# Performance work log

Hardware: AMD Instinct MI355X
Metric: run time of the kernel (lower is better)

The kernel has to match this reference:

```python
import jax, jax.numpy as jnp
import numpy as np

INPUT_SZ = 1024
HIDDEN_SZ = 1024


def setup_inputs() -> dict:
    key = jax.random.key(0)
    k1, k2, k3, k4, k5, k6 = jax.random.split(key, 6)
    s = 1.0 / np.sqrt(INPUT_SZ)
    x_batch = jax.random.normal(k1, (8, 2048, INPUT_SZ), dtype=jnp.float32)
    lin_w = jax.random.normal(k2, (INPUT_SZ, INPUT_SZ), dtype=jnp.float32) * s  # nn.Linear weight (out,in)
    lin_b = jax.random.normal(k3, (INPUT_SZ,), dtype=jnp.float32) * s
    W_q = jax.random.normal(k4, (INPUT_SZ, HIDDEN_SZ), dtype=jnp.float32) * s
    W_k = jax.random.normal(k5, (INPUT_SZ, HIDDEN_SZ), dtype=jnp.float32) * s
    W_v = jax.random.normal(k6, (INPUT_SZ, HIDDEN_SZ), dtype=jnp.float32) * s
    return {"x_batch": x_batch, "lin_w": lin_w, "lin_b": lin_b,
            "W_q": W_q, "W_k": W_k, "W_v": W_v}


def reference(x_batch, lin_w, lin_b, W_q, W_k, W_v):
    # x_batch: [B, S, D]. Prefill path (empty kv_cache of shape (2,)).
    B, S, D = x_batch.shape
    x = jnp.einsum('bsd,ed->bse', x_batch, lin_w) + lin_b  # nn.Linear: x @ W.T + b
    Q = jnp.einsum('bsd,dh->bsh', x, W_q)
    K = jnp.einsum('bsd,dh->bsh', x, W_k)
    V = jnp.einsum('bsd,dh->bsh', x, W_v)
    current_cache = jnp.stack([K, V])  # [2, B, S, H]
    I = jnp.einsum('bqh,bkh->bqk', Q, K)  # NOTE: no 1/sqrt(d) scaling, per original
    causal_mask = jnp.triu(jnp.ones((S, S), dtype=bool), k=1)  # True above diagonal
    I = jnp.where(causal_mask[None, :, :], -jnp.inf, I)
    F = jnp.einsum('bqk,bkh->bqh', jax.nn.softmax(I, axis=-1), V)
    return (F, current_cache)
```

## Files before the change

### kernel.cpp

```cpp
#include <hip/hip_runtime.h>
#include <cstdint>
#include <cstddef>
#include <cmath>


typedef short bf16x8 __attribute__((ext_vector_type(8)));
typedef float f32x4 __attribute__((ext_vector_type(4)));

__device__ __forceinline__ unsigned short f2bf(float f) {
    unsigned u = __float_as_uint(f);
    return (unsigned short)((u + 0x7fffu + ((u >> 16) & 1u)) >> 16);
}
__device__ __forceinline__ float bf2f(unsigned short h) {
    return __uint_as_float(((unsigned)h) << 16);
}

#define GLDS(gp, lp)                                                                \
    __builtin_amdgcn_global_load_lds((const __attribute__((address_space(1))) void*)(gp), \
                                     (__attribute__((address_space(3))) void*)(lp), 16, 0, 0)

#define PACK_BATCH ((size_t)136 * 16384)


__global__ __launch_bounds__(256)
void cvt_split(const float* __restrict__ in, unsigned short* __restrict__ h,
               unsigned short* __restrict__ l, size_t n4)
{
    size_t i = (size_t)blockIdx.x * blockDim.x + threadIdx.x;
    size_t stride = (size_t)gridDim.x * blockDim.x;
    for (; i < n4; i += stride) {
        float4 v = ((const float4*)in)[i];
        unsigned short h0 = f2bf(v.x), h1 = f2bf(v.y), h2 = f2bf(v.z), h3 = f2bf(v.w);
        uint2 hp, lp;
        hp.x = (unsigned)h0 | ((unsigned)h1 << 16);
        hp.y = (unsigned)h2 | ((unsigned)h3 << 16);
        lp.x = (unsigned)f2bf(v.x - bf2f(h0)) | ((unsigned)f2bf(v.y - bf2f(h1)) << 16);
        lp.y = (unsigned)f2bf(v.z - bf2f(h2)) | ((unsigned)f2bf(v.w - bf2f(h3)) << 16);
        ((uint2*)h)[i] = hp;
        ((uint2*)l)[i] = lp;
    }
}

template<bool PAIR>
__global__ __launch_bounds__(256)
void cvt_split_T(const float* __restrict__ in, unsigned short* __restrict__ hT,
                 unsigned short* __restrict__ lT, int R, int C,
                 size_t inBatch, size_t outBatch)
{
    __shared__ float tile[64][65];
    in += (size_t)blockIdx.z * inBatch;
    hT += (size_t)blockIdx.z * outBatch;
    const int c0 = blockIdx.x * 64, r0 = blockIdx.y * 64;
    const int tx = threadIdx.x & 63, ty = threadIdx.x >> 6;
    for (int i = ty; i < 64; i += 4)
        tile[i][tx] = in[(size_t)(r0 + i) * C + c0 + tx];
    __syncthreads();
    for (int i = ty; i < 64; i += 4) {
        float v = tile[tx][i];
        unsigned short hh = f2bf(v);
        size_t off = (size_t)(c0 + i) * R + r0 + tx;
        hT[off] = hh;
        if (PAIR) (lT + (size_t)blockIdx.z * outBatch)[off] = f2bf(v - bf2f(hh));
    }
}


template<bool SPLIT, bool BIAS, bool QKT, bool OUTF, bool OUTH, bool OUTL>
__global__ __launch_bounds__(512, 2)
void gemm256(const unsigned short* __restrict__ Ah, const unsigned short* __restrict__ Al,
             const unsigned short* __restrict__ Bh, const unsigned short* __restrict__ Bl,
             const float* __restrict__ bias,
             float* __restrict__ C, float* __restrict__ C7,
             unsigned short* __restrict__ Ch, unsigned short* __restrict__ Cl,
             int K, int ldA, int ldB, int ldC, int nbx,
             size_t aBatch, size_t bBatch)
{
    int row0, col0, batch = 0;
    if (QKT) {
        const int bid = blockIdx.x;
        batch = bid & 7;
        const int ti = bid >> 3;
        int r = (int)((sqrtf(8.f * (float)ti + 1.f) - 1.f) * 0.5f);
        while (((r + 1) * (r + 2)) / 2 <= ti) ++r;
        while ((r * (r + 1)) / 2 > ti) --r;
        const int c = ti - (r * (r + 1)) / 2;
        row0 = r * 256; col0 = c * 256;
        Ah += (size_t)batch * aBatch; Bh += (size_t)batch * bBatch;
        if (SPLIT) { Al += (size_t)batch * aBatch; Bl += (size_t)batch * bBatch; }
    } else {
        const int bid = blockIdx.x;
        const int chunk = gridDim.x >> 3;
        const int lb = (bid & 7) * chunk + (bid >> 3);
        row0 = (lb / nbx) * 256; col0 = (lb % nbx) * 256;
    }

    constexpr int PL = 8192;
    constexpr int BUF = SPLIT ? 32768 : 16384;
    __shared__ unsigned short sm[SPLIT ? 65536 : 32768];

    const int t = threadIdx.x, wave = t >> 6, lane = t & 63;
    const int wr = wave >> 2, wc = wave & 3;
    const int mrow = lane & 15, kg = lane >> 4;
    const int c0 = wave * 2, c1 = wave * 2 + 1;

    const size_t aOff0 = (size_t)(row0 + c0 * 16 + mrow) * ldA + kg * 8;
    const size_t aOff1 = (size_t)(row0 + c1 * 16 + mrow) * ldA + kg * 8;
    const size_t bOff0 = (size_t)(col0 + c0 * 16 + mrow) * ldB + kg * 8;
    const size_t bOff1 = (size_t)(col0 + c1 * 16 + mrow) * ldB + kg * 8;

    f32x4 acc[8][4] = {};
    const int nt = K / 32;

#define STAGE256(step, bb)                                                   \
    do {                                                                     \
        unsigned short* db = sm + (bb);                                      \
        const size_t kof = (size_t)(step) * 32;                              \
        GLDS(Ah + aOff0 + kof, db + c0 * 512);                               \
        GLDS(Ah + aOff1 + kof, db + c1 * 512);                               \
        GLDS(Bh + bOff0 + kof, db + (SPLIT ? 2 * PL : PL) + c0 * 512);       \
        GLDS(Bh + bOff1 + kof, db + (SPLIT ? 2 * PL : PL) + c1 * 512);       \
        if (SPLIT) {                                                         \
            GLDS(Al + aOff0 + kof, db + PL + c0 * 512);                      \
            GLDS(Al + aOff1 + kof, db + PL + c1 * 512);                      \
            GLDS(Bl + bOff0 + kof, db + 3 * PL + c0 * 512);                  \
            GLDS(Bl + bOff1 + kof, db + 3 * PL + c1 * 512);                  \
        }                                                                    \
    } while (0)

    STAGE256(0, 0);
    __syncthreads();

    for (int ts = 0; ts < nt; ++ts) {
        unsigned short* sb = sm + (ts & 1) * BUF;
        if (ts + 1 < nt) STAGE256(ts + 1, ((ts + 1) & 1) * BUF);
        bf16x8 bh[4], bl[4];
        #pragma unroll
        for (int j = 0; j < 4; ++j) {
            bh[j] = *(const bf16x8*)(sb + (SPLIT ? 2 * PL : PL) + (wc * 4 + j) * 512 + lane * 8);
            if (SPLIT) bl[j] = *(const bf16x8*)(sb + 3 * PL + (wc * 4 + j) * 512 + lane * 8);
        }
        #pragma unroll
        for (int i = 0; i < 8; ++i) {
            bf16x8 ah = *(const bf16x8*)(sb + (wr * 8 + i) * 512 + lane * 8);
            bf16x8 al;
            if (SPLIT) al = *(const bf16x8*)(sb + PL + (wr * 8 + i) * 512 + lane * 8);
            __builtin_amdgcn_s_setprio(1);
            #pragma unroll
            for (int j = 0; j < 4; ++j) {
                acc[i][j] = __builtin_amdgcn_mfma_f32_16x16x32_bf16(ah, bh[j], acc[i][j], 0, 0, 0);
                if (SPLIT) {
                    acc[i][j] = __builtin_amdgcn_mfma_f32_16x16x32_bf16(ah, bl[j], acc[i][j], 0, 0, 0);
                    acc[i][j] = __builtin_amdgcn_mfma_f32_16x16x32_bf16(al, bh[j], acc[i][j], 0, 0, 0);
                }
            }
            __builtin_amdgcn_s_setprio(0);
        }
        __syncthreads();
    }
#undef STAGE256

    float* Cout = C;
    if (QKT) Cout = (batch == 7) ? C7 : C + (size_t)batch * PACK_BATCH;
    const int rb = (lane >> 4) * 4, cl = lane & 15;
    #pragma unroll
    for (int j = 0; j < 4; ++j) {
        const int col = col0 + wc * 64 + j * 16 + cl;
        const float bv = BIAS ? bias[col] : 0.f;
        #pragma unroll
        for (int i = 0; i < 8; ++i) {
            const int rw = row0 + wr * 128 + i * 16 + rb;
            #pragma unroll
            for (int r = 0; r < 4; ++r) {
                const int row = rw + r;
                float v = acc[i][j][r];
                if (BIAS) v += bv;
                if (QKT) {
                    if (col > row) v = -__builtin_huge_valf();
                    const int rblk = row >> 7, cblk = col >> 7;
                    if (rblk >= cblk) {
                        const size_t off = ((size_t)(((rblk * (rblk + 1)) >> 1) + cblk) << 14)
                                         + ((size_t)(row & 127) << 7) + (size_t)(col & 127);
                        Cout[off] = v;
                    }
                } else {
                    const size_t off = (size_t)row * ldC + col;
                    if (OUTF) Cout[off] = v;
                    if (OUTH) {
                        unsigned short hh = f2bf(v);
                        Ch[off] = hh;
                        if (OUTL) Cl[off] = f2bf(v - bf2f(hh));
                    }
                }
            }
        }
    }
}


template<bool SPLIT, bool BIAS, bool CMASK, bool CK, bool OUTF, bool OUTH, bool OUTL,
         bool PACKC, bool PACKA>
__global__ __launch_bounds__(256)
void gemm_bf16(const unsigned short* __restrict__ Ah, const unsigned short* __restrict__ Al,
               const unsigned short* __restrict__ Bh, const unsigned short* __restrict__ Bl,
               const float* __restrict__ bias,
               float* __restrict__ C, float* __restrict__ C7,
               unsigned short* __restrict__ Ch, unsigned short* __restrict__ Cl,
               int K, int ldA, int ldB, int ldC,
               size_t aBatch, size_t bBatch, size_t cBatch)
{
    const int row0 = blockIdx.y * 128, col0 = blockIdx.x * 128;
    if (CMASK && col0 > row0 + 127) return;

    const int bz = blockIdx.z;
    if (aBatch) { Ah += (size_t)bz * aBatch; if (SPLIT) Al += (size_t)bz * aBatch; }
    if (bBatch) { Bh += (size_t)bz * bBatch; if (SPLIT) Bl += (size_t)bz * bBatch; }
    if (cBatch) { C += (size_t)bz * cBatch; }

    extern __shared__ __align__(16) unsigned short smd[];
    unsigned short* sAh = smd;
    unsigned short* sBh = smd + 4096;
    unsigned short* sAl = smd + 8192;
    unsigned short* sBl = smd + 12288;

    const int t = threadIdx.x;
    const int wave = t >> 6, lane = t & 63;
    const int wr = wave >> 1, wc = wave & 1;
    const int mrow = lane & 15, kg = lane >> 4;

    int kEnd = K;
    if (CK) kEnd = min(K, row0 + 128);

    f32x4 acc[4][4] = {};

    const int c0 = wave * 2, c1 = wave * 2 + 1;
    size_t aOff0, aOff1;
    if (PACKA) {
        const int rblk = row0 >> 7;
        const size_t baseA = (((size_t)bz * 136) + (size_t)((rblk * (rblk + 1)) >> 1)) << 14;
        aOff0 = baseA + (size_t)(c0 * 16 + mrow) * 128 + kg * 8;
        aOff1 = baseA + (size_t)(c1 * 16 + mrow) * 128 + kg * 8;
    } else {
        aOff0 = (size_t)(row0 + c0 * 16 + mrow) * ldA + kg * 8;
        aOff1 = (size_t)(row0 + c1 * 16 + mrow) * ldA + kg * 8;
    }
    const size_t bOff0 = (size_t)(col0 + c0 * 16 + mrow) * ldB + kg * 8;
    const size_t bOff1 = (size_t)(col0 + c1 * 16 + mrow) * ldB + kg * 8;

    for (int k0 = 0; k0 < kEnd; k0 += 32) {
        const size_t aK = PACKA ? ((((size_t)(k0 >> 7)) << 14) | (size_t)(k0 & 127))
                                : (size_t)k0;
        GLDS(Ah + aOff0 + aK, sAh + c0 * 512);
        GLDS(Ah + aOff1 + aK, sAh + c1 * 512);
        GLDS(Bh + bOff0 + k0, sBh + c0 * 512);
        GLDS(Bh + bOff1 + k0, sBh + c1 * 512);
        if (SPLIT) {
            GLDS(Al + aOff0 + aK, sAl + c0 * 512);
            GLDS(Al + aOff1 + aK, sAl + c1 * 512);
            GLDS(Bl + bOff0 + k0, sBl + c0 * 512);
            GLDS(Bl + bOff1 + k0, sBl + c1 * 512);
        }
        __syncthreads();

        bf16x8 afh[4], bfh[4], afl[4], bfl[4];
        #pragma unroll
        for (int i = 0; i < 4; ++i) {
            afh[i] = *(const bf16x8*)(sAh + (wr * 4 + i) * 512 + lane * 8);
            bfh[i] = *(const bf16x8*)(sBh + (wc * 4 + i) * 512 + lane * 8);
            if (SPLIT) {
                afl[i] = *(const bf16x8*)(sAl + (wr * 4 + i) * 512 + lane * 8);
                bfl[i] = *(const bf16x8*)(sBl + (wc * 4 + i) * 512 + lane * 8);
            }
        }
        #pragma unroll
        for (int i = 0; i < 4; ++i)
            #pragma unroll
            for (int j = 0; j < 4; ++j) {
                acc[i][j] = __builtin_amdgcn_mfma_f32_16x16x32_bf16(afh[i], bfh[j], acc[i][j], 0, 0, 0);
                if (SPLIT) {
                    acc[i][j] = __builtin_amdgcn_mfma_f32_16x16x32_bf16(afh[i], bfl[j], acc[i][j], 0, 0, 0);
                    acc[i][j] = __builtin_amdgcn_mfma_f32_16x16x32_bf16(afl[i], bfh[j], acc[i][j], 0, 0, 0);
                }
            }
        __syncthreads();
    }

    float* Cout = C;
    size_t cbase = 0;
    if (PACKC) {
        const int rblk = row0 >> 7, cblk = col0 >> 7;
        Cout = (bz == 7) ? C7 : C + (size_t)bz * PACK_BATCH;
        cbase = ((size_t)((rblk * (rblk + 1)) >> 1) + (size_t)cblk) << 14;
    }
    const int rb = (lane >> 4) * 4;
    const int cl = lane & 15;
    #pragma unroll
    for (int j = 0; j < 4; ++j) {
        const int col = col0 + wc * 64 + j * 16 + cl;
        float bv = BIAS ? bias[col] : 0.f;
        #pragma unroll
        for (int i = 0; i < 4; ++i) {
            const int rw = row0 + wr * 64 + i * 16 + rb;
            #pragma unroll
            for (int r = 0; r < 4; ++r) {
                const int row = rw + r;
                float v = acc[i][j][r];
                if (BIAS) v += bv;
                if (CMASK && col > row) v = -__builtin_huge_valf();
                const size_t off = PACKC
                    ? (cbase + (size_t)(row - row0) * 128 + (size_t)(col - col0))
                    : ((size_t)row * ldC + col);
                if (OUTF) Cout[off] = v;
                if (OUTH) {
                    unsigned short hh = f2bf(v);
                    Ch[off] = hh;
                    if (OUTL) Cl[off] = f2bf(v - bf2f(hh));
                }
            }
        }
    }
}

__global__ __launch_bounds__(256)
void softmax_p_packed(const float* __restrict__ SF, const float* __restrict__ S7,
                      unsigned short* __restrict__ P)
{
    const int q = blockIdx.x, b = blockIdx.y;
    const int rblk = q >> 7, tri = (rblk * (rblk + 1)) >> 1;
    const size_t rowoff = ((size_t)tri << 14) + (size_t)(q & 127) * 128;
    const float* rowb = ((b == 7) ? S7 : SF + (size_t)b * PACK_BATCH) + rowoff;
    unsigned short* prow = P + (size_t)b * PACK_BATCH + rowoff;
    const int kend = rblk * 128 + 128;
    const int t = threadIdx.x;
    __shared__ float red[4];

    float m = -__builtin_huge_valf();
    for (int k = t; k < kend; k += 256)
        m = fmaxf(m, rowb[(((size_t)(k >> 7)) << 14) + (k & 127)]);
    #pragma unroll
    for (int off = 32; off; off >>= 1) m = fmaxf(m, __shfl_down(m, off, 64));
    if ((t & 63) == 0) red[t >> 6] = m;
    __syncthreads();
    m = fmaxf(fmaxf(red[0], red[1]), fmaxf(red[2], red[3]));
    __syncthreads();

    float e[8];
    float s = 0.f;
    int i = 0;
    for (int k = t; k < kend; k += 256, ++i) {
        float v = __expf(rowb[(((size_t)(k >> 7)) << 14) + (k & 127)] - m);
        e[i] = v;
        s += v;
    }
    #pragma unroll
    for (int off = 32; off; off >>= 1) s += __shfl_down(s, off, 64);
    if ((t & 63) == 0) red[t >> 6] = s;
    __syncthreads();
    s = red[0] + red[1] + red[2] + red[3];
    const float inv = 1.0f / s;
    i = 0;
    for (int k = t; k < kend; k += 256, ++i)
        prow[(((size_t)(k >> 7)) << 14) + (k & 127)] = f2bf(e[i] * inv);
}

#define TILE 64
#define KT 16
#define LDP (TILE + 4)
template<bool BT, bool BIAS, bool CMASK, bool CK>
__global__ __launch_bounds__(256)
void gemm_f32(const float* __restrict__ A, const float* __restrict__ B,
              const float* __restrict__ bias, float* __restrict__ C,
              int M, int N, int K, size_t sA, size_t sB, size_t sC)
{
    const int bm = blockIdx.y, bn = blockIdx.x;
    const int row0 = bm * TILE, col0 = bn * TILE;
    if (CMASK && col0 > row0 + (TILE - 1)) return;
    A += (size_t)blockIdx.z * sA; B += (size_t)blockIdx.z * sB; C += (size_t)blockIdx.z * sC;
    __shared__ float As[KT][LDP];
    __shared__ float Bs[KT][LDP];
    const int t = threadIdx.x;
    const int tx = t & 15, ty = t >> 4;
    const int lm = t >> 2, lk = (t & 3) << 2;
    int kEnd = K;
    if (CK) kEnd = min(K, row0 + TILE);
    float acc[4][4] = {};
    for (int k0 = 0; k0 < kEnd; k0 += KT) {
        {
            float4 a = *(const float4*)(A + (size_t)(row0 + lm) * K + (k0 + lk));
            As[lk + 0][lm] = a.x; As[lk + 1][lm] = a.y; As[lk + 2][lm] = a.z; As[lk + 3][lm] = a.w;
        }
        if (BT) {
            float4 b = *(const float4*)(B + (size_t)(col0 + lm) * K + (k0 + lk));
            Bs[lk + 0][lm] = b.x; Bs[lk + 1][lm] = b.y; Bs[lk + 2][lm] = b.z; Bs[lk + 3][lm] = b.w;
        } else {
            const int bk = t >> 4, bn4 = (t & 15) << 2;
            *(float4*)&Bs[bk][bn4] = *(const float4*)(B + (size_t)(k0 + bk) * N + (col0 + bn4));
        }
        __syncthreads();
        #pragma unroll
        for (int kk = 0; kk < KT; ++kk) {
            float av[4], bv[4];
            *(float4*)av = *(const float4*)&As[kk][ty << 2];
            *(float4*)bv = *(const float4*)&Bs[kk][tx << 2];
            #pragma unroll
            for (int i = 0; i < 4; ++i)
                #pragma unroll
                for (int j = 0; j < 4; ++j) acc[i][j] = fmaf(av[i], bv[j], acc[i][j]);
        }
        __syncthreads();
    }
    #pragma unroll
    for (int i = 0; i < 4; ++i) {
        const int r = row0 + (ty << 2) + i;
        float4 o; float* po = &o.x;
        #pragma unroll
        for (int j = 0; j < 4; ++j) {
            const int c = col0 + (tx << 2) + j;
            float v = acc[i][j];
            if (BIAS) v += bias[c];
            if (CMASK && c > r) v = -__builtin_huge_valf();
            po[j] = v;
        }
        *(float4*)(C + (size_t)r * N + col0 + (tx << 2)) = o;
    }
}
__global__ __launch_bounds__(256)
void softmax_causal(float* __restrict__ Sc, size_t batchStride, int ncols)
{
    const int q = blockIdx.x;
    float* row = Sc + (size_t)blockIdx.y * batchStride + (size_t)q * ncols;
    const int kend = (q & ~63) + 64;
    const int t = threadIdx.x;
    __shared__ float red[4];
    float m = -__builtin_huge_valf();
    for (int k = t; k < kend; k += 256) m = fmaxf(m, row[k]);
    #pragma unroll
    for (int off = 32; off; off >>= 1) m = fmaxf(m, __shfl_down(m, off, 64));
    if ((t & 63) == 0) red[t >> 6] = m;
    __syncthreads();
    m = fmaxf(fmaxf(red[0], red[1]), fmaxf(red[2], red[3]));
    __syncthreads();
    float e[8]; float s = 0.f; int i = 0;
    for (int k = t; k < kend; k += 256, ++i) { float v = __expf(row[k] - m); e[i] = v; s += v; }
    #pragma unroll
    for (int off = 32; off; off >>= 1) s += __shfl_down(s, off, 64);
    if ((t & 63) == 0) red[t >> 6] = s;
    __syncthreads();
    s = red[0] + red[1] + red[2] + red[3];
    const float inv = 1.0f / s;
    i = 0;
    for (int k = t; k < kend; k += 256, ++i) row[k] = e[i] * inv;
}


extern "C" void kernel_launch(void* const* d_in, const int* in_sizes, int n_in,
                              void* d_out, int out_size, void* d_ws, size_t ws_size,
                              hipStream_t stream)
{
    const float* x_batch = (const float*)d_in[0];
    const float* lin_w   = (const float*)d_in[1];
    const float* lin_b   = (const float*)d_in[2];
    const float* W_q     = (const float*)d_in[3];
    const float* W_k     = (const float*)d_in[4];
    const float* W_v     = (const float*)d_in[5];

    constexpr int Bn = 8, S = 2048, D = 1024;
    constexpr size_t MS = (size_t)Bn * S;
    constexpr size_t NE = MS * (size_t)D;
    constexpr size_t SB = (size_t)S * D;

    float* out = (float*)d_out;
    float* Fo = out;
    float* Kc = out + NE;
    float* Vc = out + 2 * NE;

    const size_t needFast = NE * 2 * 2ull
                          + NE * 2 * 2ull
                          + 14680064ull;

    if (ws_size >= needFast) {
        unsigned short* Qh  = (unsigned short*)d_ws;
        unsigned short* Ql  = Qh + NE;
        unsigned short* Kh  = Ql + NE;
        unsigned short* Kl  = Kh + NE;
        unsigned short* X   = Kl + NE;
        unsigned short* lwh = X,            *lwl = X + 1048576;
        unsigned short* wqh = X + 2097152,  *wql = X + 3145728;
        unsigned short* wkh = X + 4194304,  *wkl = X + 5242880;
        unsigned short* wvh = X + 6291456;
        float*          S7f = (float*)X;
        float*          SF  = Fo;
        unsigned short* Ph  = Qh;
        unsigned short* VhT = Kh;

        unsigned short* xbh = (unsigned short*)Kc;
        unsigned short* xbl = xbh + NE;
        unsigned short* xh  = (unsigned short*)Fo;
        unsigned short* xl  = xh + NE;

        const dim3 blk(256);
        const dim3 blk512(512);

        cvt_split<<<4096, blk, 0, stream>>>(x_batch, xbh, xbl, NE / 4);
        cvt_split<<<512,  blk, 0, stream>>>(lin_w, lwh, lwl, (size_t)D * D / 4);
        cvt_split_T<true ><<<dim3(16, 16, 1), blk, 0, stream>>>(W_q, wqh, wql, D, D, 0, 0);
        cvt_split_T<true ><<<dim3(16, 16, 1), blk, 0, stream>>>(W_k, wkh, wkl, D, D, 0, 0);
        cvt_split_T<false><<<dim3(16, 16, 1), blk, 0, stream>>>(W_v, wvh, nullptr, D, D, 0, 0);

        gemm256<true, true, false, false, true, true><<<dim3(256), blk512, 0, stream>>>(
            xbh, xbl, lwh, lwl, lin_b, nullptr, nullptr, xh, xl, D, D, D, D, 4, 0, 0);
        gemm256<true, false, false, false, true, true><<<dim3(256), blk512, 0, stream>>>(
            xh, xl, wqh, wql, nullptr, nullptr, nullptr, Qh, Ql, D, D, D, D, 4, 0, 0);
        gemm256<true, false, false, true, true, true><<<dim3(256), blk512, 0, stream>>>(
            xh, xl, wkh, wkl, nullptr, Kc, nullptr, Kh, Kl, D, D, D, D, 4, 0, 0);
        gemm256<false, false, false, true, false, false><<<dim3(256), blk512, 0, stream>>>(
            xh, nullptr, wvh, nullptr, nullptr, Vc, nullptr, nullptr, nullptr,
            D, D, D, D, 4, 0, 0);

        gemm256<true, false, true, true, false, false><<<dim3(288), blk512, 0, stream>>>(
            Qh, Ql, Kh, Kl, nullptr, SF, S7f, nullptr, nullptr,
            D, D, D, 128, 1, SB, SB);

        softmax_p_packed<<<dim3(S, Bn), blk, 0, stream>>>(SF, S7f, Ph);

        cvt_split_T<false><<<dim3(D / 64, S / 64, Bn), blk, 0, stream>>>(
            Vc, VhT, nullptr, S, D, SB, SB);

        gemm_bf16<false, false, false, true, true, false, false, false, true>
            <<<dim3(D / 128, S / 128, Bn), blk, 16384, stream>>>(
                Ph, nullptr, VhT, nullptr, nullptr,
                Fo, nullptr, nullptr, nullptr, S, 128, S, D, 0, SB, SB);
    } else {
        float* x  = Fo;
        float* Q  = (float*)d_ws;
        float* Sc = Q + NE;
        const dim3 blk(256);
        const dim3 gBig(D / TILE, MS / TILE, 1);
        gemm_f32<true, true, false, false><<<gBig, blk, 0, stream>>>(
            x_batch, lin_w, lin_b, x, (int)MS, D, D, 0, 0, 0);
        gemm_f32<false, false, false, false><<<gBig, blk, 0, stream>>>(
            x, W_q, nullptr, Q, (int)MS, D, D, 0, 0, 0);
        gemm_f32<false, false, false, false><<<gBig, blk, 0, stream>>>(
            x, W_k, nullptr, Kc, (int)MS, D, D, 0, 0, 0);
        gemm_f32<false, false, false, false><<<gBig, blk, 0, stream>>>(
            x, W_v, nullptr, Vc, (int)MS, D, D, 0, 0, 0);
        for (int b = 0; b < Bn; ++b) {
            const float* Qb = Q  + (size_t)b * SB;
            const float* Kb = Kc + (size_t)b * SB;
            const float* Vb = Vc + (size_t)b * SB;
            float*       Fb = Fo + (size_t)b * SB;
            gemm_f32<true, false, true, false><<<dim3(S / TILE, S / TILE, 1), blk, 0, stream>>>(
                Qb, Kb, nullptr, Sc, S, S, D, 0, 0, 0);
            softmax_causal<<<dim3(S, 1, 1), blk, 0, stream>>>(Sc, 0, S);
            gemm_f32<false, false, false, true><<<dim3(D / TILE, S / TILE, 1), blk, 0, stream>>>(
                Sc, Vb, nullptr, Fb, S, D, S, 0, 0, 0);
        }
    }
}
```

Before: 1.063 ms.

## Split GEMM k-step into phases interleaving LDS reads, prefetch and MFMA with barriers

After: 1.077 ms. About the same (+1.3%).

```diff
diff --git a/kernel.cpp b/kernel.cpp
--- a/kernel.cpp
+++ b/kernel.cpp
@@ -110,54 +110,98 @@
 
     f32x4 acc[8][4] = {};
     const int nt = K / 32;
-
-#define STAGE256(step, bb)                                                   \
+    constexpr int NPH = SPLIT ? 4 : 2;
+    constexpr int RPP = 8 / NPH;
+
+#define STAGE_A(step, db)                                                    \
     do {                                                                     \
-        unsigned short* db = sm + (bb);                                      \
         const size_t kof = (size_t)(step) * 32;                              \
-        GLDS(Ah + aOff0 + kof, db + c0 * 512);                               \
-        GLDS(Ah + aOff1 + kof, db + c1 * 512);                               \
-        GLDS(Bh + bOff0 + kof, db + (SPLIT ? 2 * PL : PL) + c0 * 512);       \
-        GLDS(Bh + bOff1 + kof, db + (SPLIT ? 2 * PL : PL) + c1 * 512);       \
+        GLDS(Ah + aOff0 + kof, (db) + c0 * 512);                             \
+        GLDS(Ah + aOff1 + kof, (db) + c1 * 512);                             \
         if (SPLIT) {                                                         \
-            GLDS(Al + aOff0 + kof, db + PL + c0 * 512);                      \
-            GLDS(Al + aOff1 + kof, db + PL + c1 * 512);                      \
-            GLDS(Bl + bOff0 + kof, db + 3 * PL + c0 * 512);                  \
-            GLDS(Bl + bOff1 + kof, db + 3 * PL + c1 * 512);                  \
+            GLDS(Al + aOff0 + kof, (db) + PL + c0 * 512);                    \
+            GLDS(Al + aOff1 + kof, (db) + PL + c1 * 512);                    \
         }                                                                    \
     } while (0)
-
-    STAGE256(0, 0);
-    __syncthreads();
+#define STAGE_B(step, db)                                                    \
+    do {                                                                     \
+        const size_t kof = (size_t)(step) * 32;                              \
+        unsigned short* bp = (db) + (SPLIT ? 2 * PL : PL);                   \
+        GLDS(Bh + bOff0 + kof, bp + c0 * 512);                               \
+        GLDS(Bh + bOff1 + kof, bp + c1 * 512);                               \
+        if (SPLIT) {                                                         \
+            GLDS(Bl + bOff0 + kof, bp + PL + c0 * 512);                      \
+            GLDS(Bl + bOff1 + kof, bp + PL + c1 * 512);                      \
+        }                                                                    \
+    } while (0)
+
+    STAGE_A(0, sm);
+    STAGE_B(0, sm);
+    asm volatile("s_waitcnt vmcnt(0)" ::: "memory");
+    __builtin_amdgcn_sched_barrier(0);
+    __builtin_amdgcn_s_barrier();
+    __builtin_amdgcn_sched_barrier(0);
 
     for (int ts = 0; ts < nt; ++ts) {
         unsigned short* sb = sm + (ts & 1) * BUF;
-        if (ts + 1 < nt) STAGE256(ts + 1, ((ts + 1) & 1) * BUF);
+        unsigned short* nb = sm + ((ts + 1) & 1) * BUF;
+        const unsigned short* sA0 = sb;
+        const unsigned short* sB0 = sb + (SPLIT ? 2 * PL : PL);
+        const bool pf = (ts + 1 < nt);
+
         bf16x8 bh[4], bl[4];
         #pragma unroll
-        for (int j = 0; j < 4; ++j) {
-            bh[j] = *(const bf16x8*)(sb + (SPLIT ? 2 * PL : PL) + (wc * 4 + j) * 512 + lane * 8);
-            if (SPLIT) bl[j] = *(const bf16x8*)(sb + 3 * PL + (wc * 4 + j) * 512 + lane * 8);
-        }
-        #pragma unroll
-        for (int i = 0; i < 8; ++i) {
-            bf16x8 ah = *(const bf16x8*)(sb + (wr * 8 + i) * 512 + lane * 8);
-            bf16x8 al;
-            if (SPLIT) al = *(const bf16x8*)(sb + PL + (wr * 8 + i) * 512 + lane * 8);
+        for (int ph = 0; ph < NPH; ++ph) {
+            bf16x8 ah[RPP], al[RPP];
+            if (ph == 0) {
+                #pragma unroll
+                for (int j = 0; j < 4; ++j) {
+                    bh[j] = *(const bf16x8*)(sB0 + (wc * 4 + j) * 512 + lane * 8);
+                    if (SPLIT) bl[j] = *(const bf16x8*)(sB0 + PL + (wc * 4 + j) * 512 + lane * 8);
+                }
+            }
+            #pragma unroll
+            for (int u = 0; u < RPP; ++u) {
+                const int ri = wr * 8 + ph * RPP + u;
+                ah[u] = *(const bf16x8*)(sA0 + ri * 512 + lane * 8);
+                if (SPLIT) al[u] = *(const bf16x8*)(sA0 + PL + ri * 512 + lane * 8);
+            }
+            if (ph == 0 && pf) {
+                STAGE_A(ts + 1, nb);
+                if (!SPLIT) STAGE_B(ts + 1, nb);
+            }
+            if (SPLIT && ph == 1 && pf) STAGE_B(ts + 1, nb);
+
+            __builtin_amdgcn_sched_barrier(0);
+            __builtin_amdgcn_s_barrier();
+            asm volatile("s_waitcnt lgkmcnt(0)" ::: "memory");
+            __builtin_amdgcn_sched_barrier(0);
+
             __builtin_amdgcn_s_setprio(1);
             #pragma unroll
-            for (int j = 0; j < 4; ++j) {
-                acc[i][j] = __builtin_amdgcn_mfma_f32_16x16x32_bf16(ah, bh[j], acc[i][j], 0, 0, 0);
-                if (SPLIT) {
-                    acc[i][j] = __builtin_amdgcn_mfma_f32_16x16x32_bf16(ah, bl[j], acc[i][j], 0, 0, 0);
-                    acc[i][j] = __builtin_amdgcn_mfma_f32_16x16x32_bf16(al, bh[j], acc[i][j], 0, 0, 0);
+            for (int u = 0; u < RPP; ++u) {
+                const int i = ph * RPP + u;
+                #pragma unroll
+                for (int j = 0; j < 4; ++j) {
+                    acc[i][j] = __builtin_amdgcn_mfma_f32_16x16x32_bf16(ah[u], bh[j], acc[i][j], 0, 0, 0);
+                    if (SPLIT) {
+                        acc[i][j] = __builtin_amdgcn_mfma_f32_16x16x32_bf16(ah[u], bl[j], acc[i][j], 0, 0, 0);
+                        acc[i][j] = __builtin_amdgcn_mfma_f32_16x16x32_bf16(al[u], bh[j], acc[i][j], 0, 0, 0);
+                    }
                 }
             }
             __builtin_amdgcn_s_setprio(0);
-        }
-        __syncthreads();
-    }
-#undef STAGE256
+
+            if (ph == NPH - 1) {
+                asm volatile("s_waitcnt vmcnt(0)" ::: "memory");
+            }
+            __builtin_amdgcn_sched_barrier(0);
+            __builtin_amdgcn_s_barrier();
+            __builtin_amdgcn_sched_barrier(0);
+        }
+    }
+#undef STAGE_A
+#undef STAGE_B
 
     float* Cout = C;
     if (QKT) Cout = (batch == 7) ? C7 : C + (size_t)batch * PACK_BATCH;
```

## Prefetch two K-steps ahead with partial vmcnt waits in GEMM loop

Applied to the files above, without the earlier changes.

After: 1.125 ms. 1.06x slower.

```diff
diff --git a/kernel.cpp b/kernel.cpp
--- a/kernel.cpp
+++ b/kernel.cpp
@@ -111,39 +111,50 @@
     f32x4 acc[8][4] = {};
     const int nt = K / 32;
 
-#define STAGE256(step, bb)                                                   \
+#define STAGE256(step, db)                                                   \
     do {                                                                     \
-        unsigned short* db = sm + (bb);                                      \
         const size_t kof = (size_t)(step) * 32;                              \
-        GLDS(Ah + aOff0 + kof, db + c0 * 512);                               \
-        GLDS(Ah + aOff1 + kof, db + c1 * 512);                               \
-        GLDS(Bh + bOff0 + kof, db + (SPLIT ? 2 * PL : PL) + c0 * 512);       \
-        GLDS(Bh + bOff1 + kof, db + (SPLIT ? 2 * PL : PL) + c1 * 512);       \
+        GLDS(Ah + aOff0 + kof, (db) + c0 * 512);                             \
+        GLDS(Ah + aOff1 + kof, (db) + c1 * 512);                             \
+        GLDS(Bh + bOff0 + kof, (db) + (SPLIT ? 2 * PL : PL) + c0 * 512);     \
+        GLDS(Bh + bOff1 + kof, (db) + (SPLIT ? 2 * PL : PL) + c1 * 512);     \
         if (SPLIT) {                                                         \
-            GLDS(Al + aOff0 + kof, db + PL + c0 * 512);                      \
-            GLDS(Al + aOff1 + kof, db + PL + c1 * 512);                      \
-            GLDS(Bl + bOff0 + kof, db + 3 * PL + c0 * 512);                  \
-            GLDS(Bl + bOff1 + kof, db + 3 * PL + c1 * 512);                  \
+            GLDS(Al + aOff0 + kof, (db) + PL + c0 * 512);                    \
+            GLDS(Al + aOff1 + kof, (db) + PL + c1 * 512);                    \
+            GLDS(Bl + bOff0 + kof, (db) + 3 * PL + c0 * 512);                \
+            GLDS(Bl + bOff1 + kof, (db) + 3 * PL + c1 * 512);                \
         }                                                                    \
     } while (0)
 
-    STAGE256(0, 0);
-    __syncthreads();
+    STAGE256(0, sm);
+    if (nt > 1) STAGE256(1, sm + BUF);
 
     for (int ts = 0; ts < nt; ++ts) {
         unsigned short* sb = sm + (ts & 1) * BUF;
-        if (ts + 1 < nt) STAGE256(ts + 1, ((ts + 1) & 1) * BUF);
+        const unsigned short* sA0 = sb;
+        const unsigned short* sB0 = sb + (SPLIT ? 2 * PL : PL);
+
+        if (ts + 1 < nt) {
+            if (SPLIT) asm volatile("s_waitcnt vmcnt(8)" ::: "memory");
+            else       asm volatile("s_waitcnt vmcnt(4)" ::: "memory");
+        } else {
+            asm volatile("s_waitcnt vmcnt(0)" ::: "memory");
+        }
+        __builtin_amdgcn_sched_barrier(0);
+        __builtin_amdgcn_s_barrier();
+        __builtin_amdgcn_sched_barrier(0);
+
         bf16x8 bh[4], bl[4];
         #pragma unroll
         for (int j = 0; j < 4; ++j) {
-            bh[j] = *(const bf16x8*)(sb + (SPLIT ? 2 * PL : PL) + (wc * 4 + j) * 512 + lane * 8);
-            if (SPLIT) bl[j] = *(const bf16x8*)(sb + 3 * PL + (wc * 4 + j) * 512 + lane * 8);
+            bh[j] = *(const bf16x8*)(sB0 + (wc * 4 + j) * 512 + lane * 8);
+            if (SPLIT) bl[j] = *(const bf16x8*)(sB0 + PL + (wc * 4 + j) * 512 + lane * 8);
         }
         #pragma unroll
         for (int i = 0; i < 8; ++i) {
-            bf16x8 ah = *(const bf16x8*)(sb + (wr * 8 + i) * 512 + lane * 8);
+            bf16x8 ah = *(const bf16x8*)(sA0 + (wr * 8 + i) * 512 + lane * 8);
             bf16x8 al;
-            if (SPLIT) al = *(const bf16x8*)(sb + PL + (wr * 8 + i) * 512 + lane * 8);
+            if (SPLIT) al = *(const bf16x8*)(sA0 + PL + (wr * 8 + i) * 512 + lane * 8);
             __builtin_amdgcn_s_setprio(1);
             #pragma unroll
             for (int j = 0; j < 4; ++j) {
@@ -155,7 +166,11 @@
             }
             __builtin_amdgcn_s_setprio(0);
         }
-        __syncthreads();
+
+        __builtin_amdgcn_sched_barrier(0);
+        __builtin_amdgcn_s_barrier();
+        __builtin_amdgcn_sched_barrier(0);
+        if (ts + 2 < nt) STAGE256(ts + 2, sb);
     }
 #undef STAGE256
 
```

## Fuse V transpose into V-projection epilogue and switch projections to gemm_bf16

Applied to the files above, without the earlier changes.

Measured after the change: 1.125 ms. +5.9%, slower.

```diff
diff --git a/kernel.cpp b/kernel.cpp
--- a/kernel.cpp
+++ b/kernel.cpp
@@ -65,13 +65,14 @@
 }
 
 
-template<bool SPLIT, bool BIAS, bool QKT, bool OUTF, bool OUTH, bool OUTL>
+template<bool SPLIT, bool BIAS, bool QKT, bool OUTF, bool OUTH, bool OUTL, bool OUTT>
 __global__ __launch_bounds__(512, 2)
 void gemm256(const unsigned short* __restrict__ Ah, const unsigned short* __restrict__ Al,
              const unsigned short* __restrict__ Bh, const unsigned short* __restrict__ Bl,
              const float* __restrict__ bias,
              float* __restrict__ C, float* __restrict__ C7,
              unsigned short* __restrict__ Ch, unsigned short* __restrict__ Cl,
+             unsigned short* __restrict__ Ct,
              int K, int ldA, int ldB, int ldC, int nbx,
              size_t aBatch, size_t bBatch)
 {
@@ -133,11 +134,12 @@
     for (int ts = 0; ts < nt; ++ts) {
         unsigned short* sb = sm + (ts & 1) * BUF;
         if (ts + 1 < nt) STAGE256(ts + 1, ((ts + 1) & 1) * BUF);
+        const unsigned short* sB0 = sb + (SPLIT ? 2 * PL : PL);
         bf16x8 bh[4], bl[4];
         #pragma unroll
         for (int j = 0; j < 4; ++j) {
-            bh[j] = *(const bf16x8*)(sb + (SPLIT ? 2 * PL : PL) + (wc * 4 + j) * 512 + lane * 8);
-            if (SPLIT) bl[j] = *(const bf16x8*)(sb + 3 * PL + (wc * 4 + j) * 512 + lane * 8);
+            bh[j] = *(const bf16x8*)(sB0 + (wc * 4 + j) * 512 + lane * 8);
+            if (SPLIT) bl[j] = *(const bf16x8*)(sB0 + PL + (wc * 4 + j) * 512 + lane * 8);
         }
         #pragma unroll
         for (int i = 0; i < 8; ++i) {
@@ -169,12 +171,11 @@
         #pragma unroll
         for (int i = 0; i < 8; ++i) {
             const int rw = row0 + wr * 128 + i * 16 + rb;
-            #pragma unroll
-            for (int r = 0; r < 4; ++r) {
-                const int row = rw + r;
-                float v = acc[i][j][r];
-                if (BIAS) v += bv;
-                if (QKT) {
+            if (QKT) {
+                #pragma unroll
+                for (int r = 0; r < 4; ++r) {
+                    const int row = rw + r;
+                    float v = acc[i][j][r];
                     if (col > row) v = -__builtin_huge_valf();
                     const int rblk = row >> 7, cblk = col >> 7;
                     if (rblk >= cblk) {
@@ -182,14 +183,28 @@
                                          + ((size_t)(row & 127) << 7) + (size_t)(col & 127);
                         Cout[off] = v;
                     }
-                } else {
-                    const size_t off = (size_t)row * ldC + col;
+                }
+            } else {
+                float vv[4];
+                #pragma unroll
+                for (int r = 0; r < 4; ++r) {
+                    float v = acc[i][j][r];
+                    if (BIAS) v += bv;
+                    vv[r] = v;
+                    const size_t off = (size_t)(rw + r) * ldC + col;
                     if (OUTF) Cout[off] = v;
                     if (OUTH) {
                         unsigned short hh = f2bf(v);
                         Ch[off] = hh;
                         if (OUTL) Cl[off] = f2bf(v - bf2f(hh));
                     }
+                }
+                if (OUTT) {
+                    ushort4 u;
+                    u.x = f2bf(vv[0]); u.y = f2bf(vv[1]);
+                    u.z = f2bf(vv[2]); u.w = f2bf(vv[3]);
+                    *(ushort4*)(Ct + (((size_t)(rw >> 11)) << 21)
+                                   + ((size_t)col << 11) + (rw & 2047)) = u;
                 }
             }
         }
@@ -475,6 +490,7 @@
 
     const size_t needFast = NE * 2 * 2ull
                           + NE * 2 * 2ull
+                          + NE * 2ull
                           + 14680064ull;
 
     if (ws_size >= needFast) {
@@ -482,7 +498,8 @@
         unsigned short* Ql  = Qh + NE;
         unsigned short* Kh  = Ql + NE;
         unsigned short* Kl  = Kh + NE;
-        unsigned short* X   = Kl + NE;
+        unsigned short* VhT = Kl + NE;
+        unsigned short* X   = VhT + NE;
         unsigned short* lwh = X,            *lwl = X + 1048576;
         unsigned short* wqh = X + 2097152,  *wql = X + 3145728;
         unsigned short* wkh = X + 4194304,  *wkl = X + 5242880;
@@ -490,7 +507,6 @@
         float*          S7f = (float*)X;
         float*          SF  = Fo;
         unsigned short* Ph  = Qh;
-        unsigned short* VhT = Kh;
 
         unsigned short* xbh = (unsigned short*)Kc;
         unsigned short* xbl = xbh + NE;
@@ -506,24 +522,26 @@
         cvt_split_T<true ><<<dim3(16, 16, 1), blk, 0, stream>>>(W_k, wkh, wkl, D, D, 0, 0);
         cvt_split_T<false><<<dim3(16, 16, 1), blk, 0, stream>>>(W_v, wvh, nullptr, D, D, 0, 0);
 
-        gemm256<true, true, false, false, true, true><<<dim3(256), blk512, 0, stream>>>(
-            xbh, xbl, lwh, lwl, lin_b, nullptr, nullptr, xh, xl, D, D, D, D, 4, 0, 0);
-        gemm256<true, false, false, false, true, true><<<dim3(256), blk512, 0, stream>>>(
-            xh, xl, wqh, wql, nullptr, nullptr, nullptr, Qh, Ql, D, D, D, D, 4, 0, 0);
-        gemm256<true, false, false, true, true, true><<<dim3(256), blk512, 0, stream>>>(
-            xh, xl, wkh, wkl, nullptr, Kc, nullptr, Kh, Kl, D, D, D, D, 4, 0, 0);
-        gemm256<false, false, false, true, false, false><<<dim3(256), blk512, 0, stream>>>(
-            xh, nullptr, wvh, nullptr, nullptr, Vc, nullptr, nullptr, nullptr,
+        const dim3 gBig(D / 128, MS / 128);
+
+        gemm_bf16<true, true, false, false, false, true, true, false, false>
+            <<<gBig, blk, 32768, stream>>>(xbh, xbl, lwh, lwl, lin_b,
+                                           nullptr, nullptr, xh, xl, D, D, D, D, 0, 0, 0);
+        gemm_bf16<true, false, false, false, false, true, true, false, false>
+            <<<gBig, blk, 32768, stream>>>(xh, xl, wqh, wql, nullptr,
+                                           nullptr, nullptr, Qh, Ql, D, D, D, D, 0, 0, 0);
+        gemm_bf16<true, false, false, false, true, true, true, false, false>
+            <<<gBig, blk, 32768, stream>>>(xh, xl, wkh, wkl, nullptr,
+                                           Kc, nullptr, Kh, Kl, D, D, D, D, 0, 0, 0);
+        gemm256<false, false, false, true, false, false, true><<<dim3(256), blk512, 0, stream>>>(
+            xh, nullptr, wvh, nullptr, nullptr, Vc, nullptr, nullptr, nullptr, VhT,
             D, D, D, D, 4, 0, 0);
 
-        gemm256<true, false, true, true, false, false><<<dim3(288), blk512, 0, stream>>>(
-            Qh, Ql, Kh, Kl, nullptr, SF, S7f, nullptr, nullptr,
+        gemm256<true, false, true, true, false, false, false><<<dim3(288), blk512, 0, stream>>>(
+            Qh, Ql, Kh, Kl, nullptr, SF, S7f, nullptr, nullptr, nullptr,
             D, D, D, 128, 1, SB, SB);
 
         softmax_p_packed<<<dim3(S, Bn), blk, 0, stream>>>(SF, S7f, Ph);
-
-        cvt_split_T<false><<<dim3(D / 64, S / 64, Bn), blk, 0, stream>>>(
-            Vc, VhT, nullptr, S, D, SB, SB);
 
         gemm_bf16<false, false, false, true, true, false, false, false, true>
             <<<dim3(D / 128, S / 128, Bn), blk, 16384, stream>>>(
```
